# Kernel tuning notes

Measured on AMD Instinct MI355X. Metric: run time of the kernel, lower is better.

The kernel has to match this reference:

```python
import jax, jax.numpy as jnp
import numpy as np

B, S, D = 1, 2048, 1024
H, HD = 16, 64          # attention heads, head dim
DFF = 4096              # ffn hidden
IH, ID = 4, 64          # indexer heads / dim ('baseline' strategy)
TOP_K = 64
ROPE_BASE = 10000.0
LN_EPS = 1e-5


def setup_inputs() -> dict:
    key = jax.random.key(0)
    ks = jax.random.split(key, 12)
    g = lambda k, shape: (jax.random.normal(k, shape, dtype=jnp.float32) * 0.02)
    return {
        "x": jax.random.normal(ks[0], (B, S, D), dtype=jnp.float32),
        "w_qkv": g(ks[1], (D, 3 * D)),
        "w_o": g(ks[2], (D, D)),
        "ffn_w1": g(ks[3], (D, DFF)),
        "ffn_b1": jnp.zeros((DFF,), jnp.float32),
        "ffn_w2": g(ks[4], (DFF, D)),
        "ffn_b2": jnp.zeros((D,), jnp.float32),
        "ln1_g": jnp.ones((D,), jnp.float32),
        "ln1_b": jnp.zeros((D,), jnp.float32),
        "ln2_g": jnp.ones((D,), jnp.float32),
        "ln2_b": jnp.zeros((D,), jnp.float32),
        "idx_wq": g(ks[5], (D, IH * ID)),
        "idx_wk": g(ks[6], (D, ID)),
        "idx_ww": g(ks[7], (D, IH)),
    }


def _layernorm(x, g, b):
    m = jnp.mean(x, axis=-1, keepdims=True)
    v = jnp.var(x, axis=-1, keepdims=True)
    return (x - m) * jax.lax.rsqrt(v + LN_EPS) * g + b


def _rope(x):  # x: [B,S,H,HD], torchtune interleaved-pair convention
    half = HD // 2
    theta = 1.0 / (ROPE_BASE ** (jnp.arange(0, HD, 2, dtype=jnp.float32) / HD))  # [half]
    ang = jnp.arange(S, dtype=jnp.float32)[:, None] * theta                      # [S,half]
    cos = jnp.cos(ang)[None, :, None, :]
    sin = jnp.sin(ang)[None, :, None, :]
    xp = x.reshape(*x.shape[:-1], half, 2)
    x0, x1 = xp[..., 0], xp[..., 1]
    out = jnp.stack([x0 * cos - x1 * sin, x1 * cos + x0 * sin], axis=-1)
    return out.reshape(x.shape)


def reference(x, w_qkv, w_o, ffn_w1, ffn_b1, ffn_w2, ffn_b2,
              ln1_g, ln1_b, ln2_g, ln2_b, idx_wq, idx_wk, idx_ww):
    norm_x = _layernorm(x, ln1_g, ln1_b)

    qkv = norm_x @ w_qkv                              # [B,S,3D]
    q, k, v = jnp.split(qkv, 3, axis=-1)
    q = _rope(q.reshape(B, S, H, HD))
    k = _rope(k.reshape(B, S, H, HD))
    v = v.reshape(B, S, H, HD)

    # Lightning-style indexer: I[t,s] = sum_h w[t,h] * relu(q_i[t,h] . k_i[s])
    qi = (norm_x @ idx_wq).reshape(B, S, IH, ID)      # [B,S,IH,ID]
    ki = norm_x @ idx_wk                              # [B,S,ID]
    wi = norm_x @ idx_ww                              # [B,S,IH]
    qk = jnp.einsum("bthd,bsd->bths", qi, ki)         # [B,S,IH,S]
    index_scores = jnp.einsum("bth,bths->bts", wi, jax.nn.relu(qk))  # [B,S,S]

    # causal top-k token selection -> boolean mask
    causal = jnp.tril(jnp.ones((S, S), dtype=bool))
    masked_scores = jnp.where(causal, index_scores, -jnp.inf)
    _, topk_idx = jax.lax.top_k(masked_scores, TOP_K)  # [B,S,K]
    b_ix = jnp.arange(B)[:, None, None]
    q_ix = jnp.arange(S)[None, :, None]
    mask = jnp.zeros((B, S, S), dtype=bool).at[b_ix, q_ix, topk_idx].set(True)
    mask = mask & causal                               # [B,S,S]

    # masked SDPA
    logits = jnp.einsum("bqhd,bkhd->bhqk", q, k) / np.sqrt(HD)
    logits = jnp.where(mask[:, None, :, :], logits, -jnp.inf)
    attn = jax.nn.softmax(logits, axis=-1)
    attn_out = jnp.einsum("bhqk,bkhd->bqhd", attn, v).reshape(B, S, D)
    x = x + attn_out @ w_o

    h = _layernorm(x, ln2_g, ln2_b)
    ffn = jax.nn.gelu(h @ ffn_w1 + ffn_b1, approximate=False) @ ffn_w2 + ffn_b2
    return x + ffn
```

## Files before the change

kernel.cpp:

```cpp
#include <hip/hip_runtime.h>
#include <math.h>

#define S_LEN 2048
#define D_MODEL 1024
#define NHEAD 16
#define HDIM 64
#define DFF 4096
#define IH 4
#define IDM 64
#define TOPK 64
#define NIDX 336

typedef float f32x4 __attribute__((ext_vector_type(4)));
typedef short bf16x8 __attribute__((ext_vector_type(8)));

__device__ __forceinline__ unsigned short f2bf(float f) {
    unsigned u = __builtin_bit_cast(unsigned, f);
    u += 0x7fff + ((u >> 16) & 1);
    return (unsigned short)(u >> 16);
}
__device__ __forceinline__ float bf2f(unsigned short us) {
    return __builtin_bit_cast(float, (unsigned)us << 16);
}

__device__ __forceinline__ float gelu_exact(float v) {
    return 0.5f * v * (1.f + erff(v * 0.70710678118654752f));
}

__device__ __forceinline__ void gl_lds16(const void* g, void* l) {
    __builtin_amdgcn_global_load_lds(
        (const __attribute__((address_space(1))) void*)g,
        (__attribute__((address_space(3))) void*)l, 16, 0, 0);
}

__global__ __launch_bounds__(256) void ln_kernel(const float* __restrict__ x,
    const float* __restrict__ g, const float* __restrict__ b,
    float* __restrict__ outf, unsigned short* __restrict__ outb)
{
    int row = blockIdx.x, tid = threadIdx.x;
    const float4 v = *(const float4*)(x + (size_t)row * D_MODEL + tid * 4);
    float s = v.x + v.y + v.z + v.w;
    float ss = v.x * v.x + v.y * v.y + v.z * v.z + v.w * v.w;
    int lane = tid & 63, wv = tid >> 6;
    for (int o = 32; o; o >>= 1) { s += __shfl_xor(s, o); ss += __shfl_xor(ss, o); }
    __shared__ float rs[4], rss[4];
    if (lane == 0) { rs[wv] = s; rss[wv] = ss; }
    __syncthreads();
    float S = rs[0] + rs[1] + rs[2] + rs[3];
    float SS = rss[0] + rss[1] + rss[2] + rss[3];
    float mean = S * (1.f / D_MODEL);
    float var = SS * (1.f / D_MODEL) - mean * mean;
    float r = rsqrtf(var + 1e-5f);
    float4 gv = *(const float4*)(g + tid * 4);
    float4 bv = *(const float4*)(b + tid * 4);
    float4 o4;
    o4.x = (v.x - mean) * r * gv.x + bv.x;
    o4.y = (v.y - mean) * r * gv.y + bv.y;
    o4.z = (v.z - mean) * r * gv.z + bv.z;
    o4.w = (v.w - mean) * r * gv.w + bv.w;
    if (outf) *(float4*)(outf + (size_t)row * D_MODEL + tid * 4) = o4;
    if (outb) {
        ushort4 u4 = { f2bf(o4.x), f2bf(o4.y), f2bf(o4.z), f2bf(o4.w) };
        *(ushort4*)(outb + (size_t)row * D_MODEL + tid * 4) = u4;
    }
}

__device__ __forceinline__ void wtrans_body(const float* __restrict__ in,
    unsigned short* __restrict__ out, int K, int N, int bx, int by, int tid)
{
    __shared__ float t[32][33];
    int k0 = by * 32, n0 = bx * 32;
    int r = tid >> 5, c = tid & 31;
#pragma unroll
    for (int p = 0; p < 4; ++p)
        t[r + p * 8][c] = in[(size_t)(k0 + r + p * 8) * N + n0 + c];
    __syncthreads();
#pragma unroll
    for (int p = 0; p < 4; ++p)
        out[(size_t)(n0 + r + p * 8) * K + k0 + c] = f2bf(t[c][r + p * 8]);
}

#define PREP_ROPE   256
#define PREP_WQKV   3072
#define PREP_WO     1024
#define PREP_W1     4096
#define PREP_W2     4096
#define PREP_WPACK  1344
#define PREP_TOTAL  (PREP_ROPE + PREP_WQKV + PREP_WO + PREP_W1 + PREP_W2 + PREP_WPACK)
__global__ __launch_bounds__(256) void prep_kernel(
    const float* __restrict__ w_qkv, const float* __restrict__ w_o,
    const float* __restrict__ w1, const float* __restrict__ w2,
    const float* __restrict__ wq, const float* __restrict__ wk, const float* __restrict__ ww,
    unsigned short* __restrict__ wqkv_t, unsigned short* __restrict__ wo_t,
    unsigned short* __restrict__ w1_t, unsigned short* __restrict__ w2_t,
    float* __restrict__ Wc, float* __restrict__ ct, float* __restrict__ st)
{
    int b = blockIdx.x, tid = threadIdx.x;
    if (b < PREP_ROPE) {
        int g = b * 256 + tid;
        int t = g >> 5, i = g & 31;
        float theta = powf(10000.f, -(float)i / 32.f);
        float ang = (float)t * theta;
        ct[g] = cosf(ang);
        st[g] = sinf(ang);
        return;
    }
    b -= PREP_ROPE;
    if (b < PREP_WQKV) { wtrans_body(w_qkv, wqkv_t, 1024, 3072, b % 96, b / 96, tid); return; }
    b -= PREP_WQKV;
    if (b < PREP_WO)   { wtrans_body(w_o, wo_t, 1024, 1024, b % 32, b / 32, tid); return; }
    b -= PREP_WO;
    if (b < PREP_W1)   { wtrans_body(w1, w1_t, 1024, 4096, b % 128, b / 128, tid); return; }
    b -= PREP_W1;
    if (b < PREP_W2)   { wtrans_body(w2, w2_t, 4096, 1024, b % 32, b / 32, tid); return; }
    b -= PREP_W2;
    {
        int idx = b * 256 + tid;
        if (idx >= D_MODEL * NIDX) return;
        int r = idx / NIDX, c = idx % NIDX;
        float v = 0.f;
        if (c < 256) v = wq[r * 256 + c];
        else if (c < 320) v = wk[r * 64 + (c - 256)];
        else if (c < 324) v = ww[r * 4 + (c - 320)];
        Wc[idx] = v;
    }
}

__global__ __launch_bounds__(256) void gemm_bf16_n64(
    const unsigned short* __restrict__ A, const unsigned short* __restrict__ Bt,
    float* __restrict__ C, unsigned short* __restrict__ Cb,
    const float* __restrict__ bias, const float* __restrict__ R,
    int M, int N, int K, int act,
    float* __restrict__ P, int kchunk)
{
    __shared__ __attribute__((aligned(16))) unsigned short Bs[3][64 * 32];
    int tid = threadIdx.x;
    int bm = blockIdx.y * 128, bn = blockIdx.x * 64;
    int wid = tid >> 6, lane = tid & 63;
    int wm = wid * 32;
    const unsigned short* Ab = A + (size_t)bm * K;
    const unsigned short* Bb = Bt + (size_t)bn * K;
    f32x4 acc[2][4];
#pragma unroll
    for (int i = 0; i < 2; ++i)
#pragma unroll
        for (int j = 0; j < 4; ++j)
            acc[i][j] = (f32x4){0.f, 0.f, 0.f, 0.f};

    int kbeg = blockIdx.z * kchunk;
    int NT = kchunk >> 5;
    int fr = lane & 15, fk = (lane >> 4) * 8;
    int e0 = tid * 8;
    int r0 = e0 >> 5, c0 = e0 & 31;
    const unsigned short* Ar0 = Ab + (size_t)(wm + fr) * K + fk;
    const unsigned short* Ar1 = Ab + (size_t)(wm + 16 + fr) * K + fk;

    auto STAGE_B = [&](int kt, int buf) {
        gl_lds16(Bb + (size_t)r0 * K + kbeg + kt * 32 + c0, &Bs[buf][e0]);
    };
    auto COMPUTE = [&](int buf, bf16x8 a0, bf16x8 a1) {
        bf16x8 bfv[4];
#pragma unroll
        for (int ni = 0; ni < 4; ++ni)
            bfv[ni] = *(const bf16x8*)&Bs[buf][(ni * 16 + fr) * 32 + fk];
        __builtin_amdgcn_s_setprio(1);
#pragma unroll
        for (int ni = 0; ni < 4; ++ni) {
            acc[0][ni] = __builtin_amdgcn_mfma_f32_16x16x32_bf16(a0, bfv[ni], acc[0][ni], 0, 0, 0);
            acc[1][ni] = __builtin_amdgcn_mfma_f32_16x16x32_bf16(a1, bfv[ni], acc[1][ni], 0, 0, 0);
        }
        __builtin_amdgcn_s_setprio(0);
    };

    STAGE_B(0, 0);
    STAGE_B(1, 1);
    bf16x8 a0 = *(const bf16x8*)(Ar0 + kbeg);
    bf16x8 a1 = *(const bf16x8*)(Ar1 + kbeg);
    asm volatile("s_waitcnt vmcnt(3)" ::: "memory");
    __builtin_amdgcn_s_barrier();

    for (int kt = 0; kt < NT - 2; ++kt) {
        STAGE_B(kt + 2, (kt + 2) % 3);
        int kn = kbeg + (kt + 1) * 32;
        bf16x8 an0 = *(const bf16x8*)(Ar0 + kn);
        bf16x8 an1 = *(const bf16x8*)(Ar1 + kn);
        COMPUTE(kt % 3, a0, a1);
        a0 = an0; a1 = an1;
        asm volatile("s_waitcnt vmcnt(3)" ::: "memory");
        __builtin_amdgcn_s_barrier();
    }
    {
        int kn = kbeg + (NT - 1) * 32;
        bf16x8 an0 = *(const bf16x8*)(Ar0 + kn);
        bf16x8 an1 = *(const bf16x8*)(Ar1 + kn);
        COMPUTE((NT - 2) % 3, a0, a1);
        a0 = an0; a1 = an1;
        asm volatile("s_waitcnt vmcnt(2)" ::: "memory");
        __builtin_amdgcn_s_barrier();
        COMPUTE((NT - 1) % 3, a0, a1);
    }

    int cl = lane & 15, rh = (lane >> 4) * 4;
    if (P) {
        float* Pz = P + (size_t)blockIdx.z * M * N;
#pragma unroll
        for (int mi = 0; mi < 2; ++mi)
#pragma unroll
            for (int ni = 0; ni < 4; ++ni) {
                int col = bn + ni * 16 + cl;
#pragma unroll
                for (int r = 0; r < 4; ++r) {
                    int row = bm + wm + mi * 16 + rh + r;
                    Pz[(size_t)row * N + col] = acc[mi][ni][r];
                }
            }
        return;
    }
#pragma unroll
    for (int mi = 0; mi < 2; ++mi) {
#pragma unroll
        for (int ni = 0; ni < 4; ++ni) {
            int col = bn + ni * 16 + cl;
            float bv = bias ? bias[col] : 0.f;
#pragma unroll
            for (int r = 0; r < 4; ++r) {
                int row = bm + wm + mi * 16 + rh + r;
                float v = acc[mi][ni][r] + bv;
                if (act) v = gelu_exact(v);
                size_t off = (size_t)row * N + col;
                if (R) v += R[off];
                if (C) C[off] = v;
                if (Cb) Cb[off] = f2bf(v);
            }
        }
    }
}

__global__ __launch_bounds__(256) void kreduce_kernel(const float* __restrict__ P,
    int nslice, float* __restrict__ C, const float* __restrict__ bias,
    const float* __restrict__ R, int M, int N)
{
    size_t total4 = (size_t)M * N / 4;
    size_t stride = (size_t)gridDim.x * 256;
    for (size_t i4 = blockIdx.x * 256 + threadIdx.x; i4 < total4; i4 += stride) {
        size_t off = i4 * 4;
        float4 v = *(const float4*)(P + off);
        for (int z = 1; z < nslice; ++z) {
            float4 p = *(const float4*)(P + (size_t)z * M * N + off);
            v.x += p.x; v.y += p.y; v.z += p.z; v.w += p.w;
        }
        if (bias) {
            float4 b4 = *(const float4*)(bias + (off % N));
            v.x += b4.x; v.y += b4.y; v.z += b4.z; v.w += b4.w;
        }
        if (R) {
            float4 r4 = *(const float4*)(R + off);
            v.x += r4.x; v.y += r4.y; v.z += r4.z; v.w += r4.w;
        }
        *(float4*)(C + off) = v;
    }
}

__global__ __launch_bounds__(256) void gemm64(const float* __restrict__ A,
    const float* __restrict__ B, float* __restrict__ C,
    int M, int N, int K,
    float* __restrict__ P, int kchunk)
{
    __shared__ float As[16][68];
    __shared__ float Bs[16][68];
    int tid = threadIdx.x;
    int bm = blockIdx.y, bn = blockIdx.x;
    int tx = tid & 15, ty = tid >> 4;
    int arow = tid >> 2;
    int acol = (tid & 3) << 2;
    int brow = tid >> 4;
    int bcol = (tid & 15) << 2;
    const float* Abase = A + (size_t)(bm * 64 + arow) * K + acol;
    float c[4][4] = {};
    int kbeg = blockIdx.z * kchunk;
    int kend = kbeg + kchunk;
    for (int k0 = kbeg; k0 < kend; k0 += 16) {
        float4 av = *(const float4*)(Abase + k0);
        As[acol + 0][arow] = av.x;
        As[acol + 1][arow] = av.y;
        As[acol + 2][arow] = av.z;
        As[acol + 3][arow] = av.w;
        int gcol = bn * 64 + bcol;
        const float* Bb = B + (size_t)(k0 + brow) * N;
        float4 bv;
        if (gcol + 3 < N) {
            bv = *(const float4*)(Bb + gcol);
        } else {
            bv.x = (gcol + 0 < N) ? Bb[gcol + 0] : 0.f;
            bv.y = (gcol + 1 < N) ? Bb[gcol + 1] : 0.f;
            bv.z = (gcol + 2 < N) ? Bb[gcol + 2] : 0.f;
            bv.w = (gcol + 3 < N) ? Bb[gcol + 3] : 0.f;
        }
        *(float4*)&Bs[brow][bcol] = bv;
        __syncthreads();
#pragma unroll
        for (int kk = 0; kk < 16; ++kk) {
            float4 a4 = *(const float4*)&As[kk][ty * 4];
            float4 b4 = *(const float4*)&Bs[kk][tx * 4];
            float av4[4] = { a4.x, a4.y, a4.z, a4.w };
            float bv4[4] = { b4.x, b4.y, b4.z, b4.w };
#pragma unroll
            for (int i = 0; i < 4; ++i)
#pragma unroll
                for (int j = 0; j < 4; ++j)
                    c[i][j] += av4[i] * bv4[j];
        }
        __syncthreads();
    }
    float* Out = P ? (P + (size_t)blockIdx.z * M * N) : C;
#pragma unroll
    for (int i = 0; i < 4; ++i) {
        int row = bm * 64 + ty * 4 + i;
#pragma unroll
        for (int j = 0; j < 4; ++j) {
            int col = bn * 64 + tx * 4 + j;
            if (col < N)
                Out[(size_t)row * N + col] = c[i][j];
        }
    }
}

__global__ __launch_bounds__(512) void rope_pack_kernel(
    const unsigned short* __restrict__ qkvb,
    const float* __restrict__ ct, const float* __restrict__ st,
    unsigned short* __restrict__ Qb, unsigned short* __restrict__ Kb,
    unsigned short* __restrict__ Vb)
{
    int t = blockIdx.x, tid = threadIdx.x;
    int h = tid >> 5, i = tid & 31;
    float c = ct[t * 32 + i], s = st[t * 32 + i];
    const unsigned short* base = qkvb + (size_t)t * (3 * D_MODEL);
    ushort2 q2 = *(const ushort2*)(base + h * HDIM + 2 * i);
    float q0 = bf2f(q2.x), q1 = bf2f(q2.y);
    ushort2 qo = { f2bf(q0 * c - q1 * s), f2bf(q1 * c + q0 * s) };
    *(ushort2*)(Qb + (size_t)t * D_MODEL + h * HDIM + 2 * i) = qo;
    ushort2 k2 = *(const ushort2*)(base + D_MODEL + h * HDIM + 2 * i);
    float k0 = bf2f(k2.x), k1 = bf2f(k2.y);
    ushort2 ko = { f2bf(k0 * c - k1 * s), f2bf(k1 * c + k0 * s) };
    *(ushort2*)(Kb + ((size_t)h * S_LEN + t) * HDIM + 2 * i) = ko;
    ushort2 v2 = *(const ushort2*)(base + 2 * D_MODEL + 2 * tid);
    int vh = tid >> 5, vd = (2 * tid) & 63;
    *(ushort2*)(Vb + ((size_t)vh * S_LEN + t) * HDIM + vd) = v2;
}

__global__ __launch_bounds__(256) void scores_kernel(const float* __restrict__ QIW,
    float* __restrict__ scores)
{
    int t0 = blockIdx.y * 64, s0 = blockIdx.x * 64;
    if (s0 > t0 + 63) return;
    __shared__ float qit[64][68];
    __shared__ float kit[64][68];
    __shared__ float wis[64][4];
    int tid = threadIdx.x;
    int tx = tid & 15, ty = tid >> 4;
    int lr = tid & 63;
    int cseg = tid >> 6;
    if (tid < 64) {
        float4 w4 = *(const float4*)(QIW + (size_t)(t0 + tid) * NIDX + 320);
        wis[tid][0] = w4.x; wis[tid][1] = w4.y; wis[tid][2] = w4.z; wis[tid][3] = w4.w;
    }
    float acc[4][4] = {};
#pragma unroll
    for (int h = 0; h < 4; ++h) {
        __syncthreads();
        const float* qrow = QIW + (size_t)(t0 + lr) * NIDX + h * 64 + cseg * 16;
        const float* krow = QIW + (size_t)(s0 + lr) * NIDX + 256 + cseg * 16;
#pragma unroll
        for (int q4 = 0; q4 < 4; ++q4) {
            int d = cseg * 16 + q4 * 4;
            float4 v = *(const float4*)(qrow + q4 * 4);
            qit[d + 0][lr] = v.x; qit[d + 1][lr] = v.y;
            qit[d + 2][lr] = v.z; qit[d + 3][lr] = v.w;
            if (h == 0) {
                float4 u = *(const float4*)(krow + q4 * 4);
                kit[d + 0][lr] = u.x; kit[d + 1][lr] = u.y;
                kit[d + 2][lr] = u.z; kit[d + 3][lr] = u.w;
            }
        }
        __syncthreads();
        float dot[4][4] = {};
#pragma unroll 8
        for (int d = 0; d < 64; ++d) {
            float4 a4 = *(const float4*)&qit[d][ty * 4];
            float4 b4 = *(const float4*)&kit[d][tx * 4];
            float av[4] = { a4.x, a4.y, a4.z, a4.w };
            float bv[4] = { b4.x, b4.y, b4.z, b4.w };
#pragma unroll
            for (int i = 0; i < 4; ++i)
#pragma unroll
                for (int j = 0; j < 4; ++j)
                    dot[i][j] += av[i] * bv[j];
        }
#pragma unroll
        for (int i = 0; i < 4; ++i) {
            float w = wis[ty * 4 + i][h];
#pragma unroll
            for (int j = 0; j < 4; ++j)
                acc[i][j] += w * fmaxf(dot[i][j], 0.f);
        }
    }
#pragma unroll
    for (int i = 0; i < 4; ++i) {
        float4 o4 = { acc[i][0], acc[i][1], acc[i][2], acc[i][3] };
        *(float4*)&scores[(size_t)(t0 + ty * 4 + i) * S_LEN + s0 + tx * 4] = o4;
    }
}

__global__ __launch_bounds__(256) void topk_kernel(const float* __restrict__ scores,
    int* __restrict__ topidx, int* __restrict__ topcnt)
{
    int t = blockIdx.x, tid = threadIdx.x;
    int n = t + 1;
    if (n <= TOPK) {
        if (tid < n) topidx[t * TOPK + tid] = tid;
        if (tid == 0) topcnt[t] = n;
        return;
    }
    __shared__ unsigned sc[S_LEN];
    __shared__ unsigned hist[256];
    __shared__ int selbin_s;
    __shared__ int cnt_out;
    __shared__ unsigned wsum[4];
    for (int j = tid; j < n; j += 256) {
        unsigned u = __builtin_bit_cast(unsigned, scores[(size_t)t * S_LEN + j]);
        sc[j] = (u & 0x80000000u) ? ~u : (u | 0x80000000u);
    }
    if (tid == 0) cnt_out = 0;
    int lane = tid & 63, wv = tid >> 6;
    unsigned prefix = 0;
    int kk = TOPK;
#pragma unroll
    for (int round = 0; round < 4; ++round) {
        int shift_pref = 32 - 8 * round;
        int shift_bin = 24 - 8 * round;
        hist[tid] = 0;
        __syncthreads();
        for (int j = tid; j < n; j += 256) {
            unsigned v = sc[j];
            if ((((unsigned long long)(v ^ prefix)) >> shift_pref) == 0)
                atomicAdd(&hist[(v >> shift_bin) & 0xff], 1u);
        }
        __syncthreads();
        if (wv == 0) {
            unsigned h0 = hist[4 * lane], h1 = hist[4 * lane + 1];
            unsigned h2 = hist[4 * lane + 2], h3 = hist[4 * lane + 3];
            unsigned s3 = h3, s2 = h2 + s3, s1 = h1 + s2, s0 = h0 + s1;
            unsigned acc = s0;
            for (int off = 1; off < 64; off <<= 1) {
                unsigned o = __shfl_down(acc, off);
                if (lane + off < 64) acc += o;
            }
            unsigned above = acc - s0;
            hist[4 * lane]     = s0 + above;
            hist[4 * lane + 1] = s1 + above;
            hist[4 * lane + 2] = s2 + above;
            hist[4 * lane + 3] = s3 + above;
        }
        __syncthreads();
        {
            unsigned sufb = hist[tid];
            unsigned sufn = (tid < 255) ? hist[tid + 1] : 0u;
            if (sufb >= (unsigned)kk && sufn < (unsigned)kk)
                selbin_s = tid;
        }
        __syncthreads();
        int b = selbin_s;
        unsigned above = (b < 255) ? hist[b + 1] : 0u;
        kk -= (int)above;
        prefix |= ((unsigned)b) << shift_bin;
        __syncthreads();
    }
    unsigned T = prefix;
    int chunk = (n + 255) >> 8;
    int jb = tid * chunk;
    int je = jb + chunk; if (je > n) je = n;
    int ties = 0;
    for (int j = jb; j < je; ++j) {
        unsigned v = sc[j];
        if (v > T) { int o = atomicAdd(&cnt_out, 1); topidx[t * TOPK + o] = j; }
        else if (v == T) ++ties;
    }
    unsigned inc = (unsigned)ties;
    for (int off = 1; off < 64; off <<= 1) {
        unsigned o = __shfl_up(inc, off);
        if (lane >= off) inc += o;
    }
    if (lane == 63) wsum[wv] = inc;
    __syncthreads();
    unsigned woff = 0;
    for (int w = 0; w < wv; ++w) woff += wsum[w];
    int rank = (int)(woff + inc) - ties;
    for (int j = jb; j < je && rank < kk; ++j) {
        if (sc[j] == T) {
            int o = atomicAdd(&cnt_out, 1);
            topidx[t * TOPK + o] = j;
            ++rank;
        }
    }
    if (tid == 0) topcnt[t] = TOPK;
}

__global__ __launch_bounds__(256) void attn_kernel(
    const unsigned short* __restrict__ Qb, const unsigned short* __restrict__ Kb,
    const unsigned short* __restrict__ Vb,
    const int* __restrict__ topidx, const int* __restrict__ topcnt,
    unsigned short* __restrict__ out)
{
    int t = blockIdx.x, tid = threadIdx.x;
    __shared__ int sel[TOPK];
    if (tid < TOPK) sel[tid] = topidx[t * TOPK + tid];
    __syncthreads();
    int cnt = topcnt[t];
    int lane = tid & 63, wv = tid >> 6;
    int h = blockIdx.y * 4 + wv;
    int klo = lane >> 3, oct = lane & 7;
    int rows[8];
    bool valid[8];
#pragma unroll
    for (int kg = 0; kg < 8; ++kg) {
        int k = kg * 8 + klo;
        valid[kg] = (k < cnt);
        rows[kg] = sel[valid[kg] ? k : 0];
    }
    bf16x8 q8 = *(const bf16x8*)(Qb + (size_t)t * D_MODEL + h * HDIM + oct * 8);
    float qf[8];
#pragma unroll
    for (int e = 0; e < 8; ++e) qf[e] = bf2f((unsigned short)q8[e]);

    const unsigned short* kbase = Kb + (size_t)h * S_LEN * HDIM + oct * 8;
    float p[8];
#pragma unroll
    for (int kg = 0; kg < 8; ++kg) {
        bf16x8 k8 = *(const bf16x8*)(kbase + (size_t)rows[kg] * HDIM);
        float d = 0.f;
#pragma unroll
        for (int e = 0; e < 8; ++e)
            d += bf2f((unsigned short)k8[e]) * qf[e];
        d += __shfl_xor(d, 1);
        d += __shfl_xor(d, 2);
        d += __shfl_xor(d, 4);
        p[kg] = valid[kg] ? d * 0.125f : -INFINITY;
    }
    float m = p[0];
#pragma unroll
    for (int kg = 1; kg < 8; ++kg) m = fmaxf(m, p[kg]);
    m = fmaxf(m, __shfl_xor(m, 8));
    m = fmaxf(m, __shfl_xor(m, 16));
    m = fmaxf(m, __shfl_xor(m, 32));
    float sum = 0.f;
#pragma unroll
    for (int kg = 0; kg < 8; ++kg) { p[kg] = __expf(p[kg] - m); sum += p[kg]; }
    sum += __shfl_xor(sum, 8);
    sum += __shfl_xor(sum, 16);
    sum += __shfl_xor(sum, 32);
    float rs = 1.f / sum;
    const unsigned short* vbase = Vb + (size_t)h * S_LEN * HDIM + oct * 8;
    float facc[8] = {};
#pragma unroll
    for (int kg = 0; kg < 8; ++kg) {
        bf16x8 v8 = *(const bf16x8*)(vbase + (size_t)rows[kg] * HDIM);
        float pw = p[kg] * rs;
#pragma unroll
        for (int e = 0; e < 8; ++e)
            facc[e] += pw * bf2f((unsigned short)v8[e]);
    }
#pragma unroll
    for (int e = 0; e < 8; ++e) {
        facc[e] += __shfl_xor(facc[e], 8);
        facc[e] += __shfl_xor(facc[e], 16);
        facc[e] += __shfl_xor(facc[e], 32);
    }
    if (klo == 0) {
        ushort4 o0 = { f2bf(facc[0]), f2bf(facc[1]), f2bf(facc[2]), f2bf(facc[3]) };
        ushort4 o1 = { f2bf(facc[4]), f2bf(facc[5]), f2bf(facc[6]), f2bf(facc[7]) };
        *(ushort4*)(out + (size_t)t * D_MODEL + h * HDIM + oct * 8) = o0;
        *(ushort4*)(out + (size_t)t * D_MODEL + h * HDIM + oct * 8 + 4) = o1;
    }
}

extern "C" void kernel_launch(void* const* d_in, const int* in_sizes, int n_in,
                              void* d_out, int out_size, void* d_ws, size_t ws_size,
                              hipStream_t stream)
{
    const float* x      = (const float*)d_in[0];
    const float* w_qkv  = (const float*)d_in[1];
    const float* w_o    = (const float*)d_in[2];
    const float* ffn_w1 = (const float*)d_in[3];
    const float* ffn_b1 = (const float*)d_in[4];
    const float* ffn_w2 = (const float*)d_in[5];
    const float* ffn_b2 = (const float*)d_in[6];
    const float* ln1_g  = (const float*)d_in[7];
    const float* ln1_b  = (const float*)d_in[8];
    const float* ln2_g  = (const float*)d_in[9];
    const float* ln2_b  = (const float*)d_in[10];
    const float* idx_wq = (const float*)d_in[11];
    const float* idx_wk = (const float*)d_in[12];
    const float* idx_ww = (const float*)d_in[13];
    float* outp = (float*)d_out;

    const size_t MB = 1ull << 20;
    char* ws = (char*)d_ws;
    float*          normx    = (float*)(ws + 0);
    unsigned short* attno_bf = (unsigned short*)(ws + 0);
    float*          Pf2      = (float*)(ws + 0);
    unsigned short* normx_bf = (unsigned short*)(ws + 8 * MB);
    unsigned short* h2_bf    = normx_bf;
    unsigned short* qkv_bf   = (unsigned short*)(ws + 12 * MB);
    int*            topidx   = (int*)(ws + 12 * MB);
    int*            topcnt   = (int*)(ws + 12 * MB + 512 * 1024);
    unsigned short* wqkv_t   = (unsigned short*)(ws + 24 * MB);
    unsigned short* wo_t     = (unsigned short*)(ws + 30 * MB);
    unsigned short* w1_t     = (unsigned short*)(ws + 32 * MB);
    unsigned short* w2_t     = (unsigned short*)(ws + 40 * MB);
    unsigned short* Qb       = (unsigned short*)(ws + 48 * MB);
    unsigned short* Kb       = (unsigned short*)(ws + 52 * MB);
    unsigned short* Vb       = (unsigned short*)(ws + 56 * MB);
    float*          ctab     = (float*)(ws + 60 * MB);
    float*          stab     = (float*)(ws + 60 * MB + 256 * 1024);
    float*          P_idx    = (float*)(ws + 60 * MB);
    float*          scoresb  = (float*)(ws + 60 * MB);
    float*          Pwo      = (float*)(ws + 60 * MB);
    unsigned short* ffn1_bf  = (unsigned short*)(ws + 60 * MB);
    float*          QIW      = (float*)(ws + 76 * MB);
    float*          Wc       = (float*)(ws + 79 * MB);

    dim3 blk256(256);
    auto g64n = [](int N, int M) { return dim3(N / 64, M / 128); };

    ln_kernel<<<S_LEN, blk256, 0, stream>>>(x, ln1_g, ln1_b, normx, normx_bf);
    prep_kernel<<<PREP_TOTAL, blk256, 0, stream>>>(w_qkv, w_o, ffn_w1, ffn_w2,
        idx_wq, idx_wk, idx_ww, wqkv_t, wo_t, w1_t, w2_t, Wc, ctab, stab);
    gemm_bf16_n64<<<g64n(3 * D_MODEL, S_LEN), blk256, 0, stream>>>(normx_bf, wqkv_t,
        nullptr, qkv_bf, nullptr, nullptr, S_LEN, 3 * D_MODEL, D_MODEL, 0, nullptr, D_MODEL);
    rope_pack_kernel<<<S_LEN, dim3(512), 0, stream>>>(qkv_bf, ctab, stab, Qb, Kb, Vb);
    gemm64<<<dim3((NIDX + 63) / 64, S_LEN / 64, 4), blk256, 0, stream>>>(normx, Wc,
        nullptr, S_LEN, NIDX, D_MODEL, P_idx, D_MODEL / 4);
    kreduce_kernel<<<1024, blk256, 0, stream>>>(P_idx, 4, QIW, nullptr, nullptr, S_LEN, NIDX);
    scores_kernel<<<dim3(32, 32), blk256, 0, stream>>>(QIW, scoresb);
    topk_kernel<<<S_LEN, blk256, 0, stream>>>(scoresb, topidx, topcnt);
    attn_kernel<<<dim3(S_LEN, 4), blk256, 0, stream>>>(Qb, Kb, Vb, topidx, topcnt, attno_bf);
    gemm_bf16_n64<<<dim3(D_MODEL / 64, S_LEN / 128, 2), blk256, 0, stream>>>(attno_bf, wo_t,
        nullptr, nullptr, nullptr, nullptr, S_LEN, D_MODEL, D_MODEL, 0, Pwo, D_MODEL / 2);
    kreduce_kernel<<<1024, blk256, 0, stream>>>(Pwo, 2, outp, nullptr, x, S_LEN, D_MODEL);
    ln_kernel<<<S_LEN, blk256, 0, stream>>>(outp, ln2_g, ln2_b, nullptr, h2_bf);
    gemm_bf16_n64<<<g64n(DFF, S_LEN), blk256, 0, stream>>>(h2_bf, w1_t,
        nullptr, ffn1_bf, ffn_b1, nullptr, S_LEN, DFF, D_MODEL, 1, nullptr, D_MODEL);
    gemm_bf16_n64<<<dim3(D_MODEL / 64, S_LEN / 128, 4), blk256, 0, stream>>>(ffn1_bf, w2_t,
        nullptr, nullptr, nullptr, nullptr, S_LEN, D_MODEL, DFF, 0, Pf2, DFF / 4);
    kreduce_kernel<<<1024, blk256, 0, stream>>>(Pf2, 4, outp, ffn_b2, outp, S_LEN, D_MODEL);
}
```

Before: 282.4 us.

## Stage A tiles through LDS, merge QKV and indexer GEMMs, fuse Wo reduce with LN2

```diff
diff --git a/kernel.cpp b/kernel.cpp
--- a/kernel.cpp
+++ b/kernel.cpp
@@ -65,6 +65,43 @@
     }
 }
 
+__global__ __launch_bounds__(256) void wo_ln2_kernel(const float* __restrict__ Pwo,
+    const float* __restrict__ x, const float* __restrict__ g, const float* __restrict__ b,
+    float* __restrict__ outf, unsigned short* __restrict__ outb)
+{
+    int row = blockIdx.x, tid = threadIdx.x;
+    size_t MN = (size_t)S_LEN * D_MODEL;
+    size_t off = (size_t)row * D_MODEL + tid * 4;
+    float4 p0 = *(const float4*)(Pwo + off);
+    float4 p1 = *(const float4*)(Pwo + MN + off);
+    float4 xr = *(const float4*)(x + off);
+    float4 v;
+    v.x = p0.x + p1.x + xr.x;
+    v.y = p0.y + p1.y + xr.y;
+    v.z = p0.z + p1.z + xr.z;
+    v.w = p0.w + p1.w + xr.w;
+    *(float4*)(outf + off) = v;
+    float s = v.x + v.y + v.z + v.w;
+    float ss = v.x * v.x + v.y * v.y + v.z * v.z + v.w * v.w;
+    int lane = tid & 63, wv = tid >> 6;
+    for (int o = 32; o; o >>= 1) { s += __shfl_xor(s, o); ss += __shfl_xor(ss, o); }
+    __shared__ float rs[4], rss[4];
+    if (lane == 0) { rs[wv] = s; rss[wv] = ss; }
+    __syncthreads();
+    float S = rs[0] + rs[1] + rs[2] + rs[3];
+    float SS = rss[0] + rss[1] + rss[2] + rss[3];
+    float mean = S * (1.f / D_MODEL);
+    float var = SS * (1.f / D_MODEL) - mean * mean;
+    float r = rsqrtf(var + 1e-5f);
+    float4 gv = *(const float4*)(g + tid * 4);
+    float4 bv = *(const float4*)(b + tid * 4);
+    ushort4 u4 = { f2bf((v.x - mean) * r * gv.x + bv.x),
+                   f2bf((v.y - mean) * r * gv.y + bv.y),
+                   f2bf((v.z - mean) * r * gv.z + bv.z),
+                   f2bf((v.w - mean) * r * gv.w + bv.w) };
+    *(ushort4*)(outb + off) = u4;
+}
+
 __device__ __forceinline__ void wtrans_body(const float* __restrict__ in,
     unsigned short* __restrict__ out, int K, int N, int bx, int by, int tid)
 {
@@ -133,6 +170,7 @@
     int M, int N, int K, int act,
     float* __restrict__ P, int kchunk)
 {
+    __shared__ __attribute__((aligned(16))) unsigned short As[3][128 * 32];
     __shared__ __attribute__((aligned(16))) unsigned short Bs[3][64 * 32];
     int tid = threadIdx.x;
     int bm = blockIdx.y * 128, bn = blockIdx.x * 64;
@@ -152,53 +190,44 @@
     int fr = lane & 15, fk = (lane >> 4) * 8;
     int e0 = tid * 8;
     int r0 = e0 >> 5, c0 = e0 & 31;
-    const unsigned short* Ar0 = Ab + (size_t)(wm + fr) * K + fk;
-    const unsigned short* Ar1 = Ab + (size_t)(wm + 16 + fr) * K + fk;
-
-    auto STAGE_B = [&](int kt, int buf) {
-        gl_lds16(Bb + (size_t)r0 * K + kbeg + kt * 32 + c0, &Bs[buf][e0]);
+
+    auto STAGE = [&](int kt, int buf) {
+        int k0 = kbeg + kt * 32;
+        gl_lds16(Ab + (size_t)r0 * K + k0 + c0, &As[buf][e0]);
+        gl_lds16(Ab + (size_t)(r0 + 64) * K + k0 + c0, &As[buf][e0 + 2048]);
+        gl_lds16(Bb + (size_t)r0 * K + k0 + c0, &Bs[buf][e0]);
     };
-    auto COMPUTE = [&](int buf, bf16x8 a0, bf16x8 a1) {
-        bf16x8 bfv[4];
+    auto COMPUTE = [&](int buf) {
+        bf16x8 af[2], bfv[4];
+#pragma unroll
+        for (int mi = 0; mi < 2; ++mi)
+            af[mi] = *(const bf16x8*)&As[buf][(wm + mi * 16 + fr) * 32 + fk];
 #pragma unroll
         for (int ni = 0; ni < 4; ++ni)
             bfv[ni] = *(const bf16x8*)&Bs[buf][(ni * 16 + fr) * 32 + fk];
-        __builtin_amdgcn_s_setprio(1);
-#pragma unroll
-        for (int ni = 0; ni < 4; ++ni) {
-            acc[0][ni] = __builtin_amdgcn_mfma_f32_16x16x32_bf16(a0, bfv[ni], acc[0][ni], 0, 0, 0);
-            acc[1][ni] = __builtin_amdgcn_mfma_f32_16x16x32_bf16(a1, bfv[ni], acc[1][ni], 0, 0, 0);
-        }
-        __builtin_amdgcn_s_setprio(0);
+#pragma unroll
+        for (int mi = 0; mi < 2; ++mi)
+#pragma unroll
+            for (int ni = 0; ni < 4; ++ni)
+                acc[mi][ni] = __builtin_amdgcn_mfma_f32_16x16x32_bf16(
+                    af[mi], bfv[ni], acc[mi][ni], 0, 0, 0);
     };
 
-    STAGE_B(0, 0);
-    STAGE_B(1, 1);
-    bf16x8 a0 = *(const bf16x8*)(Ar0 + kbeg);
-    bf16x8 a1 = *(const bf16x8*)(Ar1 + kbeg);
+    STAGE(0, 0);
+    STAGE(1, 1);
     asm volatile("s_waitcnt vmcnt(3)" ::: "memory");
     __builtin_amdgcn_s_barrier();
 
     for (int kt = 0; kt < NT - 2; ++kt) {
-        STAGE_B(kt + 2, (kt + 2) % 3);
-        int kn = kbeg + (kt + 1) * 32;
-        bf16x8 an0 = *(const bf16x8*)(Ar0 + kn);
-        bf16x8 an1 = *(const bf16x8*)(Ar1 + kn);
-        COMPUTE(kt % 3, a0, a1);
-        a0 = an0; a1 = an1;
+        STAGE(kt + 2, (kt + 2) % 3);
+        COMPUTE(kt % 3);
         asm volatile("s_waitcnt vmcnt(3)" ::: "memory");
         __builtin_amdgcn_s_barrier();
     }
-    {
-        int kn = kbeg + (NT - 1) * 32;
-        bf16x8 an0 = *(const bf16x8*)(Ar0 + kn);
-        bf16x8 an1 = *(const bf16x8*)(Ar1 + kn);
-        COMPUTE((NT - 2) % 3, a0, a1);
-        a0 = an0; a1 = an1;
-        asm volatile("s_waitcnt vmcnt(2)" ::: "memory");
-        __builtin_amdgcn_s_barrier();
-        COMPUTE((NT - 1) % 3, a0, a1);
-    }
+    COMPUTE((NT - 2) % 3);
+    asm volatile("s_waitcnt vmcnt(0)" ::: "memory");
+    __builtin_amdgcn_s_barrier();
+    COMPUTE((NT - 1) % 3);
 
     int cl = lane & 15, rh = (lane >> 4) * 4;
     if (P) {
@@ -236,6 +265,143 @@
     }
 }
 
+#define DUAL_QKV 768
+__global__ __launch_bounds__(256) void dual_qkv_idx_kernel(
+    const unsigned short* __restrict__ A, const unsigned short* __restrict__ Bt,
+    unsigned short* __restrict__ Cb,
+    const float* __restrict__ Af, const float* __restrict__ Bf, float* __restrict__ P)
+{
+    __shared__ __attribute__((aligned(16))) unsigned char ldsbuf[36864];
+    int b = blockIdx.x, tid = threadIdx.x;
+    if (b < DUAL_QKV) {
+        const int K = D_MODEL, N = 3 * D_MODEL;
+        unsigned short (*As)[128 * 32] = (unsigned short (*)[128 * 32])ldsbuf;
+        unsigned short (*Bs)[64 * 32] = (unsigned short (*)[64 * 32])(ldsbuf + 3 * 128 * 32 * 2);
+        int bx = b % 48, by = b / 48;
+        int bm = by * 128, bn = bx * 64;
+        int wid = tid >> 6, lane = tid & 63;
+        int wm = wid * 32;
+        const unsigned short* Ab = A + (size_t)bm * K;
+        const unsigned short* Bb = Bt + (size_t)bn * K;
+        f32x4 acc[2][4];
+#pragma unroll
+        for (int i = 0; i < 2; ++i)
+#pragma unroll
+            for (int j = 0; j < 4; ++j)
+                acc[i][j] = (f32x4){0.f, 0.f, 0.f, 0.f};
+        int NT = K >> 5;
+        int fr = lane & 15, fk = (lane >> 4) * 8;
+        int e0 = tid * 8;
+        int r0 = e0 >> 5, c0 = e0 & 31;
+        auto STAGE = [&](int kt, int buf) {
+            int k0 = kt * 32;
+            gl_lds16(Ab + (size_t)r0 * K + k0 + c0, &As[buf][e0]);
+            gl_lds16(Ab + (size_t)(r0 + 64) * K + k0 + c0, &As[buf][e0 + 2048]);
+            gl_lds16(Bb + (size_t)r0 * K + k0 + c0, &Bs[buf][e0]);
+        };
+        auto COMPUTE = [&](int buf) {
+            bf16x8 af[2], bfv[4];
+#pragma unroll
+            for (int mi = 0; mi < 2; ++mi)
+                af[mi] = *(const bf16x8*)&As[buf][(wm + mi * 16 + fr) * 32 + fk];
+#pragma unroll
+            for (int ni = 0; ni < 4; ++ni)
+                bfv[ni] = *(const bf16x8*)&Bs[buf][(ni * 16 + fr) * 32 + fk];
+#pragma unroll
+            for (int mi = 0; mi < 2; ++mi)
+#pragma unroll
+                for (int ni = 0; ni < 4; ++ni)
+                    acc[mi][ni] = __builtin_amdgcn_mfma_f32_16x16x32_bf16(
+                        af[mi], bfv[ni], acc[mi][ni], 0, 0, 0);
+        };
+        STAGE(0, 0);
+        STAGE(1, 1);
+        asm volatile("s_waitcnt vmcnt(3)" ::: "memory");
+        __builtin_amdgcn_s_barrier();
+        for (int kt = 0; kt < NT - 2; ++kt) {
+            STAGE(kt + 2, (kt + 2) % 3);
+            COMPUTE(kt % 3);
+            asm volatile("s_waitcnt vmcnt(3)" ::: "memory");
+            __builtin_amdgcn_s_barrier();
+        }
+        COMPUTE((NT - 2) % 3);
+        asm volatile("s_waitcnt vmcnt(0)" ::: "memory");
+        __builtin_amdgcn_s_barrier();
+        COMPUTE((NT - 1) % 3);
+        int cl = lane & 15, rh = (lane >> 4) * 4;
+#pragma unroll
+        for (int mi = 0; mi < 2; ++mi)
+#pragma unroll
+            for (int ni = 0; ni < 4; ++ni) {
+                int col = bn + ni * 16 + cl;
+#pragma unroll
+                for (int r = 0; r < 4; ++r) {
+                    int row = bm + wm + mi * 16 + rh + r;
+                    Cb[(size_t)row * N + col] = f2bf(acc[mi][ni][r]);
+                }
+            }
+    } else {
+        const int M = S_LEN, N = NIDX, K = D_MODEL, kchunk = D_MODEL / 4;
+        float (*As)[68] = (float (*)[68])ldsbuf;
+        float (*Bs)[68] = (float (*)[68])(ldsbuf + 16 * 68 * 4);
+        int b2 = b - DUAL_QKV;
+        int bn = b2 % 6, bm = (b2 / 6) % 32, bz = b2 / 192;
+        int tx = tid & 15, ty = tid >> 4;
+        int arow = tid >> 2;
+        int acol = (tid & 3) << 2;
+        int brow = tid >> 4;
+        int bcol = (tid & 15) << 2;
+        const float* Abase = Af + (size_t)(bm * 64 + arow) * K + acol;
+        float c[4][4] = {};
+        int kbeg = bz * kchunk;
+        int kend = kbeg + kchunk;
+        for (int k0 = kbeg; k0 < kend; k0 += 16) {
+            float4 av = *(const float4*)(Abase + k0);
+            As[acol + 0][arow] = av.x;
+            As[acol + 1][arow] = av.y;
+            As[acol + 2][arow] = av.z;
+            As[acol + 3][arow] = av.w;
+            int gcol = bn * 64 + bcol;
+            const float* Bb = Bf + (size_t)(k0 + brow) * N;
+            float4 bv;
+            if (gcol + 3 < N) {
+                bv = *(const float4*)(Bb + gcol);
+            } else {
+                bv.x = (gcol + 0 < N) ? Bb[gcol + 0] : 0.f;
+                bv.y = (gcol + 1 < N) ? Bb[gcol + 1] : 0.f;
+                bv.z = (gcol + 2 < N) ? Bb[gcol + 2] : 0.f;
+                bv.w = (gcol + 3 < N) ? Bb[gcol + 3] : 0.f;
+            }
+            *(float4*)&Bs[brow][bcol] = bv;
+            __syncthreads();
+#pragma unroll
+            for (int kk = 0; kk < 16; ++kk) {
+                float4 a4 = *(const float4*)&As[kk][ty * 4];
+                float4 b4 = *(const float4*)&Bs[kk][tx * 4];
+                float av4[4] = { a4.x, a4.y, a4.z, a4.w };
+                float bv4[4] = { b4.x, b4.y, b4.z, b4.w };
+#pragma unroll
+                for (int i = 0; i < 4; ++i)
+#pragma unroll
+                    for (int j = 0; j < 4; ++j)
+                        c[i][j] += av4[i] * bv4[j];
+            }
+            __syncthreads();
+        }
+        float* Out = P + (size_t)bz * M * N;
+#pragma unroll
+        for (int i = 0; i < 4; ++i) {
+            int row = bm * 64 + ty * 4 + i;
+#pragma unroll
+            for (int j = 0; j < 4; ++j) {
+                int col = bn * 64 + tx * 4 + j;
+                if (col < N)
+                    Out[(size_t)row * N + col] = c[i][j];
+            }
+        }
+    }
+}
+
 __global__ __launch_bounds__(256) void kreduce_kernel(const float* __restrict__ P,
     int nslice, float* __restrict__ C, const float* __restrict__ bias,
     const float* __restrict__ R, int M, int N)
@@ -258,70 +424,6 @@
             v.x += r4.x; v.y += r4.y; v.z += r4.z; v.w += r4.w;
         }
         *(float4*)(C + off) = v;
-    }
-}
-
-__global__ __launch_bounds__(256) void gemm64(const float* __restrict__ A,
-    const float* __restrict__ B, float* __restrict__ C,
-    int M, int N, int K,
-    float* __restrict__ P, int kchunk)
-{
-    __shared__ float As[16][68];
-    __shared__ float Bs[16][68];
-    int tid = threadIdx.x;
-    int bm = blockIdx.y, bn = blockIdx.x;
-    int tx = tid & 15, ty = tid >> 4;
-    int arow = tid >> 2;
-    int acol = (tid & 3) << 2;
-    int brow = tid >> 4;
-    int bcol = (tid & 15) << 2;
-    const float* Abase = A + (size_t)(bm * 64 + arow) * K + acol;
-    float c[4][4] = {};
-    int kbeg = blockIdx.z * kchunk;
-    int kend = kbeg + kchunk;
-    for (int k0 = kbeg; k0 < kend; k0 += 16) {
-        float4 av = *(const float4*)(Abase + k0);
-        As[acol + 0][arow] = av.x;
-        As[acol + 1][arow] = av.y;
-        As[acol + 2][arow] = av.z;
-        As[acol + 3][arow] = av.w;
-        int gcol = bn * 64 + bcol;
-        const float* Bb = B + (size_t)(k0 + brow) * N;
-        float4 bv;
-        if (gcol + 3 < N) {
-            bv = *(const float4*)(Bb + gcol);
-        } else {
-            bv.x = (gcol + 0 < N) ? Bb[gcol + 0] : 0.f;
-            bv.y = (gcol + 1 < N) ? Bb[gcol + 1] : 0.f;
-            bv.z = (gcol + 2 < N) ? Bb[gcol + 2] : 0.f;
-            bv.w = (gcol + 3 < N) ? Bb[gcol + 3] : 0.f;
-        }
-        *(float4*)&Bs[brow][bcol] = bv;
-        __syncthreads();
-#pragma unroll
-        for (int kk = 0; kk < 16; ++kk) {
-            float4 a4 = *(const float4*)&As[kk][ty * 4];
-            float4 b4 = *(const float4*)&Bs[kk][tx * 4];
-            float av4[4] = { a4.x, a4.y, a4.z, a4.w };
-            float bv4[4] = { b4.x, b4.y, b4.z, b4.w };
-#pragma unroll
-            for (int i = 0; i < 4; ++i)
-#pragma unroll
-                for (int j = 0; j < 4; ++j)
-                    c[i][j] += av4[i] * bv4[j];
-        }
-        __syncthreads();
-    }
-    float* Out = P ? (P + (size_t)blockIdx.z * M * N) : C;
-#pragma unroll
-    for (int i = 0; i < 4; ++i) {
-        int row = bm * 64 + ty * 4 + i;
-#pragma unroll
-        for (int j = 0; j < 4; ++j) {
-            int col = bn * 64 + tx * 4 + j;
-            if (col < N)
-                Out[(size_t)row * N + col] = c[i][j];
-        }
     }
 }
 
@@ -617,12 +719,12 @@
     unsigned short* wo_t     = (unsigned short*)(ws + 30 * MB);
     unsigned short* w1_t     = (unsigned short*)(ws + 32 * MB);
     unsigned short* w2_t     = (unsigned short*)(ws + 40 * MB);
+    float*          P_idx    = (float*)(ws + 48 * MB);
     unsigned short* Qb       = (unsigned short*)(ws + 48 * MB);
     unsigned short* Kb       = (unsigned short*)(ws + 52 * MB);
     unsigned short* Vb       = (unsigned short*)(ws + 56 * MB);
     float*          ctab     = (float*)(ws + 60 * MB);
     float*          stab     = (float*)(ws + 60 * MB + 256 * 1024);
-    float*          P_idx    = (float*)(ws + 60 * MB);
     float*          scoresb  = (float*)(ws + 60 * MB);
     float*          Pwo      = (float*)(ws + 60 * MB);
     unsigned short* ffn1_bf  = (unsigned short*)(ws + 60 * MB);
@@ -635,19 +737,16 @@
     ln_kernel<<<S_LEN, blk256, 0, stream>>>(x, ln1_g, ln1_b, normx, normx_bf);
     prep_kernel<<<PREP_TOTAL, blk256, 0, stream>>>(w_qkv, w_o, ffn_w1, ffn_w2,
         idx_wq, idx_wk, idx_ww, wqkv_t, wo_t, w1_t, w2_t, Wc, ctab, stab);
-    gemm_bf16_n64<<<g64n(3 * D_MODEL, S_LEN), blk256, 0, stream>>>(normx_bf, wqkv_t,
-        nullptr, qkv_bf, nullptr, nullptr, S_LEN, 3 * D_MODEL, D_MODEL, 0, nullptr, D_MODEL);
+    dual_qkv_idx_kernel<<<DUAL_QKV + 768, blk256, 0, stream>>>(normx_bf, wqkv_t, qkv_bf,
+        normx, Wc, P_idx);
+    kreduce_kernel<<<1024, blk256, 0, stream>>>(P_idx, 4, QIW, nullptr, nullptr, S_LEN, NIDX);
     rope_pack_kernel<<<S_LEN, dim3(512), 0, stream>>>(qkv_bf, ctab, stab, Qb, Kb, Vb);
-    gemm64<<<dim3((NIDX + 63) / 64, S_LEN / 64, 4), blk256, 0, stream>>>(normx, Wc,
-        nullptr, S_LEN, NIDX, D_MODEL, P_idx, D_MODEL / 4);
-    kreduce_kernel<<<1024, blk256, 0, stream>>>(P_idx, 4, QIW, nullptr, nullptr, S_LEN, NIDX);
     scores_kernel<<<dim3(32, 32), blk256, 0, stream>>>(QIW, scoresb);
     topk_kernel<<<S_LEN, blk256, 0, stream>>>(scoresb, topidx, topcnt);
     attn_kernel<<<dim3(S_LEN, 4), blk256, 0, stream>>>(Qb, Kb, Vb, topidx, topcnt, attno_bf);
     gemm_bf16_n64<<<dim3(D_MODEL / 64, S_LEN / 128, 2), blk256, 0, stream>>>(attno_bf, wo_t,
         nullptr, nullptr, nullptr, nullptr, S_LEN, D_MODEL, D_MODEL, 0, Pwo, D_MODEL / 2);
-    kreduce_kernel<<<1024, blk256, 0, stream>>>(Pwo, 2, outp, nullptr, x, S_LEN, D_MODEL);
-    ln_kernel<<<S_LEN, blk256, 0, stream>>>(outp, ln2_g, ln2_b, nullptr, h2_bf);
+    wo_ln2_kernel<<<S_LEN, blk256, 0, stream>>>(Pwo, x, ln2_g, ln2_b, outp, h2_bf);
     gemm_bf16_n64<<<g64n(DFF, S_LEN), blk256, 0, stream>>>(h2_bf, w1_t,
         nullptr, ffn1_bf, ffn_b1, nullptr, S_LEN, DFF, D_MODEL, 1, nullptr, D_MODEL);
     gemm_bf16_n64<<<dim3(D_MODEL / 64, S_LEN / 128, 4), blk256, 0, stream>>>(ffn1_bf, w2_t,
```

New measurement: 265.4 us. 1.06x faster.
